# Performance work log

Hardware: AMD Instinct MI355X
Metric: run time of the kernel (lower is better)

The kernel has to match this reference:

```python
import jax, jax.numpy as jnp
import numpy as np

# ---- static config (matches init_kwargs) ----
BATCH = 8; SEQ_LEN = 1024; ENC_IN = 7; PRED_LEN = 96
D_MODEL = 512; N_HEADS = 8; D_HEAD = D_MODEL // N_HEADS
D_FF = 2048; E_LAYERS = 2; FACTOR = 5
PATCH = 16; STRIDE = 8; PAD = 8
N_PATCH = (SEQ_LEN + PAD - PATCH) // STRIDE + 1  # 128
NF = D_MODEL * N_PATCH


def _sin_pe(n, d):
    # sinusoidal positional embedding (Informer/TSLib PositionalEmbedding)
    pos = np.arange(n, dtype=np.float32)[:, None]
    div = np.exp(np.arange(0, d, 2, dtype=np.float32) * (-np.log(10000.0) / d))
    pe = np.zeros((n, d), dtype=np.float32)
    pe[:, 0::2] = np.sin(pos * div)
    pe[:, 1::2] = np.cos(pos * div)
    return jnp.asarray(pe)


def _ln(x, g, b, eps=1e-5):
    m = x.mean(-1, keepdims=True)
    v = x.var(-1, keepdims=True)
    return (x - m) / jnp.sqrt(v + eps) * g + b


def _prob_attention(q, k, v, layer_idx):
    # Informer ProbAttention, mask_flag=False. q,k,v: [B,H,L,Dh]
    B, H, L, Dh = q.shape
    u = min(int(FACTOR * np.ceil(np.log(L))), L)  # sample_k == n_top here (L_Q == L_K)
    skey = jax.random.fold_in(jax.random.key(42), layer_idx)
    samp = jax.random.randint(skey, (L, u), 0, L)          # random keys per query
    k_s = k[:, :, samp, :]                                  # [B,H,L,u,Dh]
    qk_s = jnp.einsum('bhld,bhlsd->bhls', q, k_s)           # sampled scores
    M = qk_s.max(-1) - qk_s.mean(-1)                        # sparsity measure [B,H,L]
    top = jax.lax.top_k(M, u)[1]                            # active query idx [B,H,u]
    q_r = jnp.take_along_axis(q, top[..., None], axis=2)    # [B,H,u,Dh]
    scores = jnp.einsum('bhud,bhld->bhul', q_r, k) / jnp.sqrt(jnp.asarray(Dh, q.dtype))
    attn = jax.nn.softmax(scores, axis=-1)
    upd = jnp.einsum('bhul,bhld->bhud', attn, v)            # [B,H,u,Dh]
    ctx = jnp.broadcast_to(v.mean(axis=2, keepdims=True), (B, H, L, Dh))
    bi = jnp.arange(B)[:, None, None]
    hi = jnp.arange(H)[None, :, None]
    ctx = ctx.at[bi, hi, top].set(upd)                      # scatter updated queries
    return ctx


def reference(x_enc, x_mark_enc, x_dec, x_mark_dec, patch_W,
              Wq, bq, Wk, bk, Wv, bv, Wo, bo,
              c1W, c1b, c2W, c2b, ln1g, ln1b, ln2g, ln2b,
              encg, encb, headW, headb):
    B, L, C = x_enc.shape
    # Normalize('Stat'): per-series mean/std over time
    mean = x_enc.mean(axis=1, keepdims=True)
    std = jnp.sqrt(x_enc.var(axis=1, keepdims=True) + 1e-5)
    xn = (x_enc - mean) / std
    # PatchEmbedding: [B,C,L] -> replication-pad -> unfold -> linear + pos emb
    xc = jnp.pad(xn.transpose(0, 2, 1), ((0, 0), (0, 0), (0, PAD)), mode='edge')
    idx = np.arange(N_PATCH)[:, None] * STRIDE + np.arange(PATCH)
    tok = xc[:, :, idx].reshape(B * C, N_PATCH, PATCH) @ patch_W.T  # [BC,N,dm]
    tok = tok + _sin_pe(N_PATCH, D_MODEL)
    # Transformer encoder with ProbAttention
    for l in range(E_LAYERS):
        Beff, N, _ = tok.shape
        q = (tok @ Wq[l].T + bq[l]).reshape(Beff, N, N_HEADS, D_HEAD).transpose(0, 2, 1, 3)
        k = (tok @ Wk[l].T + bk[l]).reshape(Beff, N, N_HEADS, D_HEAD).transpose(0, 2, 1, 3)
        v = (tok @ Wv[l].T + bv[l]).reshape(Beff, N, N_HEADS, D_HEAD).transpose(0, 2, 1, 3)
        ctx = _prob_attention(q, k, v, l).transpose(0, 2, 1, 3).reshape(Beff, N, D_MODEL)
        x1 = _ln(tok + ctx @ Wo[l].T + bo[l], ln1g[l], ln1b[l])
        y = jax.nn.gelu(x1 @ c1W[l].T + c1b[l], approximate=False)  # conv1d k=1 == linear
        y = y @ c2W[l].T + c2b[l]
        tok = _ln(x1 + y, ln2g[l], ln2b[l])
    tok = _ln(tok, encg, encb)
    # FlattenHead: [B,C,N,dm] -> [B,C,dm,N] -> flatten -> linear -> [B,pred,C]
    feat = tok.reshape(B, C, N_PATCH, D_MODEL).transpose(0, 1, 3, 2).reshape(B, C, NF)
    dec = (feat @ headW.T + headb).transpose(0, 2, 1)
    return dec * std + mean  # de-normalize


def setup_inputs():
    key = jax.random.key(0)
    ks = iter(jax.random.split(key, 40))
    def rn(shape, s=0.02):
        return jax.random.normal(next(ks), shape, jnp.float32) * s
    return {
        'x_enc': jax.random.normal(next(ks), (BATCH, SEQ_LEN, ENC_IN), jnp.float32),
        'x_mark_enc': jax.random.normal(next(ks), (BATCH, SEQ_LEN, 4), jnp.float32),
        'x_dec': jax.random.normal(next(ks), (BATCH, 144, ENC_IN), jnp.float32),
        'x_mark_dec': jax.random.normal(next(ks), (BATCH, 144, 4), jnp.float32),
        'patch_W': rn((D_MODEL, PATCH)),
        'Wq': rn((E_LAYERS, D_MODEL, D_MODEL)), 'bq': jnp.zeros((E_LAYERS, D_MODEL)),
        'Wk': rn((E_LAYERS, D_MODEL, D_MODEL)), 'bk': jnp.zeros((E_LAYERS, D_MODEL)),
        'Wv': rn((E_LAYERS, D_MODEL, D_MODEL)), 'bv': jnp.zeros((E_LAYERS, D_MODEL)),
        'Wo': rn((E_LAYERS, D_MODEL, D_MODEL)), 'bo': jnp.zeros((E_LAYERS, D_MODEL)),
        'c1W': rn((E_LAYERS, D_FF, D_MODEL)), 'c1b': jnp.zeros((E_LAYERS, D_FF)),
        'c2W': rn((E_LAYERS, D_MODEL, D_FF)), 'c2b': jnp.zeros((E_LAYERS, D_MODEL)),
        'ln1g': jnp.ones((E_LAYERS, D_MODEL)), 'ln1b': jnp.zeros((E_LAYERS, D_MODEL)),
        'ln2g': jnp.ones((E_LAYERS, D_MODEL)), 'ln2b': jnp.zeros((E_LAYERS, D_MODEL)),
        'encg': jnp.ones((D_MODEL,)), 'encb': jnp.zeros((D_MODEL,)),
        'headW': rn((PRED_LEN, NF)), 'headb': jnp.zeros((PRED_LEN,)),
    }
```

## Files before the change

kernel.cpp:

```cpp
#include <hip/hip_runtime.h>
#include <math.h>
#include <stdint.h>

#define SEQ   1024
#define CIN   7
#define NB    8
#define BC    56
#define NP    128
#define DM    512
#define NH    8
#define DH    64
#define DFF   2048
#define U     25
#define NTOK  (BC*NP)
#define PE_COEF (-9.210340371976184f / 512.0f)
#define HKB   256
#define HNB   256

typedef __attribute__((ext_vector_type(8))) short short8;
typedef __attribute__((ext_vector_type(4))) float f32x4;

__device__ __forceinline__ short f2bf(float x) {
    union { float f; uint32_t u; } v; v.f = x;
    uint32_t r = v.u + 0x7FFFu + ((v.u >> 16) & 1u);
    return (short)(r >> 16);
}
__device__ __forceinline__ float bf2f(short x) {
    union { uint32_t u; float f; } v; v.u = ((uint32_t)(uint16_t)x) << 16;
    return v.f;
}

__device__ __forceinline__ void gl_lds16(const void* g, void* s) {
    __builtin_amdgcn_global_load_lds((const __attribute__((address_space(1))) void*)g,
                                     (__attribute__((address_space(3))) void*)s, 16, 0, 0);
}

__global__ void stats_kernel(const float* __restrict__ x, float* __restrict__ mean,
                             float* __restrict__ stdv) {
    int bc = blockIdx.x; int b = bc / CIN, c = bc % CIN;
    const float* base = x + (size_t)b * SEQ * CIN + c;
    float s = 0.f, ss = 0.f;
    for (int i = threadIdx.x; i < SEQ; i += 256) {
        float v = base[(size_t)i * CIN];
        s += v; ss += v * v;
    }
    __shared__ float rs[256], rss[256];
    rs[threadIdx.x] = s; rss[threadIdx.x] = ss; __syncthreads();
    for (int o = 128; o > 0; o >>= 1) {
        if (threadIdx.x < o) { rs[threadIdx.x] += rs[threadIdx.x + o]; rss[threadIdx.x] += rss[threadIdx.x + o]; }
        __syncthreads();
    }
    if (threadIdx.x == 0) {
        float m = rs[0] / SEQ;
        float v = rss[0] / SEQ - m * m;
        mean[bc] = m;
        stdv[bc] = sqrtf(v + 1e-5f);
    }
}

__device__ __forceinline__ void tf_round(uint32_t& x0, uint32_t& x1, uint32_t r) {
    x0 += x1; x1 = (x1 << r) | (x1 >> (32u - r)); x1 ^= x0;
}
__device__ void threefry2x32(uint32_t k0, uint32_t k1, uint32_t x0, uint32_t x1,
                             uint32_t& o0, uint32_t& o1) {
    uint32_t ks[3] = { k0, k1, k0 ^ k1 ^ 0x1BD11BDAu };
    x0 += ks[0]; x1 += ks[1];
    const uint32_t rotA[4] = {13u, 15u, 26u, 6u}, rotB[4] = {17u, 29u, 16u, 24u};
    #pragma unroll
    for (int i = 0; i < 5; i++) {
        const uint32_t* rr = (i & 1) ? rotB : rotA;
        tf_round(x0, x1, rr[0]); tf_round(x0, x1, rr[1]);
        tf_round(x0, x1, rr[2]); tf_round(x0, x1, rr[3]);
        x0 += ks[(i + 1) % 3];
        x1 += ks[(i + 2) % 3] + (uint32_t)(i + 1);
    }
    o0 = x0; o1 = x1;
}

__global__ void prep_weights(const float* __restrict__ Wq, const float* __restrict__ Wk,
                             const float* __restrict__ Wv, const float* __restrict__ bq,
                             const float* __restrict__ bk, const float* __restrict__ bv,
                             const float* __restrict__ Wo, const float* __restrict__ c1W,
                             const float* __restrict__ c2W,
                             short* __restrict__ wqkv, float* __restrict__ bqkv,
                             short* __restrict__ wo_b, short* __restrict__ c1w_b,
                             short* __restrict__ c2w_b, int* __restrict__ samp) {
    int blk = blockIdx.x, tid = threadIdx.x;
    if (blk < 1536) {
        int idx = blk * 256 + tid;
        int k4 = idx & 127;
        int n  = (idx >> 7) % 1536;
        int l  = idx / (1536 * 128);
        int sel3 = n >> 9;
        int nn = n & 511;
        const float* src = sel3 == 0 ? Wq : sel3 == 1 ? Wk : Wv;
        float4 v = *(const float4*)(src + ((size_t)l * DM + nn) * DM + k4 * 4);
        short4 o; o.x = f2bf(v.x); o.y = f2bf(v.y); o.z = f2bf(v.z); o.w = f2bf(v.w);
        *(short4*)(wqkv + ((size_t)l * 1536 + n) * DM + k4 * 4) = o;
        if (k4 == 0) {
            const float* bsrc = sel3 == 0 ? bq : sel3 == 1 ? bk : bv;
            bqkv[l * 1536 + n] = bsrc[l * DM + nn];
        }
    } else if (blk < 6144) {
        const float* in; short* out; int i;
        if (blk < 2048)      { in = Wo;  out = wo_b;  i = (blk - 1536) * 256 + tid; }
        else if (blk < 4096) { in = c1W; out = c1w_b; i = (blk - 2048) * 256 + tid; }
        else                 { in = c2W; out = c2w_b; i = (blk - 4096) * 256 + tid; }
        float4 v = ((const float4*)in)[i];
        short4 o; o.x = f2bf(v.x); o.y = f2bf(v.y); o.z = f2bf(v.z); o.w = f2bf(v.w);
        ((short4*)out)[i] = o;
    } else {
        int l = blk - 6144;
        uint32_t s0, s1; threefry2x32(0u, 42u, 0u, (uint32_t)l, s0, s1);
        uint32_t a0, a1, b0, b1;
        threefry2x32(s0, s1, 0u, 2u, a0, a1);
        threefry2x32(s0, s1, 1u, 3u, b0, b1);
        uint32_t k20 = a1, k21 = b1;
        for (int i = tid; i < 1600; i += 256) {
            uint32_t o0, o1;
            threefry2x32(k20, k21, (uint32_t)i, (uint32_t)(1600 + i), o0, o1);
            samp[l * 3200 + i]        = (int)(o0 & 127u);
            samp[l * 3200 + 1600 + i] = (int)(o1 & 127u);
        }
    }
}

__global__ void patch_embed(const float* __restrict__ x, const float* __restrict__ pw,
                            const float* __restrict__ mean, const float* __restrict__ stdv,
                            float* __restrict__ tok, short* __restrict__ tokb) {
    int p = blockIdx.x, bc = blockIdx.y;
    int b = bc / CIN, c = bc % CIN;
    __shared__ float xs[16];
    if (threadIdx.x < 16) {
        int i = p * 8 + threadIdx.x;
        if (i > SEQ - 1) i = SEQ - 1;
        xs[threadIdx.x] = (x[(size_t)b * SEQ * CIN + (size_t)i * CIN + c] - mean[bc]) / stdv[bc];
    }
    __syncthreads();
    for (int d = threadIdx.x; d < DM; d += blockDim.x) {
        float acc = 0.f;
        const float* wr = pw + d * 16;
        #pragma unroll
        for (int t = 0; t < 16; t++) acc += xs[t] * wr[t];
        int k2 = d & ~1;
        float ang = (float)p * expf((float)k2 * PE_COEF);
        acc += (d & 1) ? cosf(ang) : sinf(ang);
        size_t idx = ((size_t)bc * NP + p) * DM + d;
        tok[idx] = acc;
        tokb[idx] = f2bf(acc);
    }
}

template<int ACT, int OBF>
__global__ __launch_bounds__(256) void gemm_mfma(const short* __restrict__ A,
                                                 const short* __restrict__ W,
                                                 const float* __restrict__ bias,
                                                 float* __restrict__ Cf,
                                                 short* __restrict__ Cb,
                                                 int M, int N, int K) {
    __shared__ short LDSU[2][16384];
    int tid = threadIdx.x;
    int w = tid >> 6, lane = tid & 63;
    int row0 = blockIdx.x * 128, col0 = blockIdx.y * 128;
    int wrow = (w >> 1) * 64, wcol = (w & 1) * 64;
    int ksub = K / gridDim.z;
    int k0 = blockIdx.z * ksub;
    int nt = ksub >> 6;
    f32x4 acc[4][4] = {};

    auto stage = [&](int b, int kt) {
        #pragma unroll
        for (int i = 0; i < 4; i++) {
            int L = i * 4096 + w * 1024 + lane * 16;
            int row = L >> 7;
            int cb  = L & 127;
            int scb = cb ^ ((row & 7) << 4);
            gl_lds16(A + (size_t)(row0 + row) * K + kt + (scb >> 1),
                     (char*)&LDSU[b][0] + i * 4096 + w * 1024);
            gl_lds16(W + (size_t)(col0 + row) * K + kt + (scb >> 1),
                     (char*)&LDSU[b][8192] + i * 4096 + w * 1024);
        }
    };

    stage(0, k0);
    __syncthreads();
    int cur = 0;
    for (int t = 0; t < nt; t++) {
        if (t + 1 < nt) stage(cur ^ 1, k0 + (t + 1) * 64);
        const char* Ab = (const char*)&LDSU[cur][0];
        const char* Bb = (const char*)&LDSU[cur][8192];
        #pragma unroll
        for (int ks = 0; ks < 2; ks++) {
            int cb = ks * 64 + ((lane >> 4) << 4);
            short8 af[4], bfr[4];
            #pragma unroll
            for (int m = 0; m < 4; m++) {
                int r = wrow + m * 16 + (lane & 15);
                af[m] = *(const short8*)(Ab + r * 128 + (cb ^ ((r & 7) << 4)));
            }
            #pragma unroll
            for (int n = 0; n < 4; n++) {
                int r = wcol + n * 16 + (lane & 15);
                bfr[n] = *(const short8*)(Bb + r * 128 + (cb ^ ((r & 7) << 4)));
            }
            #pragma unroll
            for (int m = 0; m < 4; m++)
                #pragma unroll
                for (int n = 0; n < 4; n++)
                    acc[m][n] = __builtin_amdgcn_mfma_f32_16x16x32_bf16(af[m], bfr[n], acc[m][n], 0, 0, 0);
        }
        __syncthreads();
        cur ^= 1;
    }

    float* Cfo = Cf + (size_t)blockIdx.z * M * N;
    #pragma unroll
    for (int m = 0; m < 4; m++) {
        int rbase = row0 + wrow + m * 16 + ((lane >> 4) << 2);
        #pragma unroll
        for (int n = 0; n < 4; n++) {
            int col = col0 + wcol + n * 16 + (lane & 15);
            float bval = (blockIdx.z == 0) ? bias[col] : 0.f;
            #pragma unroll
            for (int j = 0; j < 4; j++) {
                float v = acc[m][n][j] + bval;
                if (ACT == 1) {
                    float u = 0.7978845608f * (v + 0.044715f * v * v * v);
                    float e = exp2f(2.8853900817779268f * u);
                    v = v - v / (e + 1.0f);
                }
                if (OBF) Cb[(size_t)(rbase + j) * N + col] = f2bf(v);
                else     Cfo[(size_t)(rbase + j) * N + col] = v;
            }
        }
    }
}

__global__ __launch_bounds__(256, 2) void attn_fused(const short* __restrict__ qkvb,
                                                     const int* __restrict__ samp,
                                                     short* __restrict__ ctxb) {
    __shared__ float Sbuf[64 * 130];
    __shared__ short Vt[64 * 128];
    __shared__ short Kls[128 * 64];
    __shared__ float Mv[128];
    __shared__ int   topl[32];
    __shared__ float vmean[64];
    __shared__ float vpart[256];

    float* Stop = Sbuf;
    short* Pb   = (short*)(Sbuf + 32 * 130);

    int bh = blockIdx.x, bc = bh >> 3, h = bh & 7;
    int tid = threadIdx.x, w = tid >> 6, lane = tid & 63;
    const short* base = qkvb + (size_t)bc * NP * 1536 + h * DH;
    short* cbase = ctxb + (size_t)bc * NP * DM + h * DH;

    for (int e = tid; e < 1024; e += 256) {
        int row = e >> 3, c8 = e & 7;
        short8 kv = *(const short8*)(base + (size_t)row * 1536 + 512 + c8 * 8);
        *(short8*)((char*)Kls + row * 128 + ((c8 * 16) ^ ((row & 7) << 4))) = kv;
        short8 vv = *(const short8*)(base + (size_t)row * 1536 + 1024 + c8 * 8);
        #pragma unroll
        for (int j = 0; j < 8; j++) {
            int d = c8 * 8 + j;
            *(short*)((char*)Vt + d * 256 + ((2 * row) ^ ((d & 7) << 4))) = vv[j];
        }
    }
    __syncthreads();
    {
        int d = tid & 63, part = tid >> 6;
        float s = 0.f;
        #pragma unroll
        for (int i4 = 0; i4 < 4; i4++) {
            short8 v = *(const short8*)((char*)Vt + d * 256 + ((part * 64 + i4 * 16) ^ ((d & 7) << 4)));
            #pragma unroll
            for (int j = 0; j < 8; j++) s += bf2f(v[j]);
        }
        vpart[part * 64 + d] = s;
    }

    for (int half = 0; half < 2; half++) {
        int ar = half * 64 + 16 * w + (lane & 15);
        const short* qp = base + (size_t)ar * 1536;
        short8 a0 = *(const short8*)(qp + (lane >> 4) * 8);
        short8 a1 = *(const short8*)(qp + 32 + (lane >> 4) * 8);
        #pragma unroll 2
        for (int ct = 0; ct < 8; ct++) {
            int br = ct * 16 + (lane & 15);
            int cb0 = (lane >> 4) * 16;
            short8 b0 = *(const short8*)((char*)Kls + br * 128 + (cb0 ^ ((br & 7) << 4)));
            short8 b1 = *(const short8*)((char*)Kls + br * 128 + ((cb0 + 64) ^ ((br & 7) << 4)));
            f32x4 acc = {};
            acc = __builtin_amdgcn_mfma_f32_16x16x32_bf16(a0, b0, acc, 0, 0, 0);
            acc = __builtin_amdgcn_mfma_f32_16x16x32_bf16(a1, b1, acc, 0, 0, 0);
            int r0 = 16 * w + ((lane >> 4) << 2);
            int c = ct * 16 + (lane & 15);
            #pragma unroll
            for (int j = 0; j < 4; j++) Sbuf[(r0 + j) * 130 + c] = acc[j] * 0.125f;
        }
        __syncthreads();
        if (tid < 64) {
            int r = half * 64 + tid;
            const int* sp = samp + r * U;
            const float* Srow = &Sbuf[tid * 130];
            float mx = -1e30f, sm = 0.f;
            #pragma unroll
            for (int s = 0; s < U; s++) { float v = Srow[sp[s]]; mx = fmaxf(mx, v); sm += v; }
            Mv[r] = mx - sm * (1.0f / U);
        } else if (half == 0 && tid < 128) {
            int d = tid - 64;
            vmean[d] = (vpart[d] + vpart[64 + d] + vpart[128 + d] + vpart[192 + d]) * (1.0f / 128.0f);
        }
        __syncthreads();
    }

    if (w == 0) {
        float v0 = Mv[lane], v1 = Mv[lane + 64];
        for (int it = 0; it < U; it++) {
            float bv; int bi;
            if (v1 > v0) { bv = v1; bi = lane + 64; } else { bv = v0; bi = lane; }
            #pragma unroll
            for (int o = 32; o > 0; o >>= 1) {
                float ov = __shfl_xor(bv, o);
                int   oi = __shfl_xor(bi, o);
                if (ov > bv || (ov == bv && oi < bi)) { bv = ov; bi = oi; }
            }
            if (lane == 0) topl[it] = bi;
            if (bi == lane) v0 = -1e30f;
            if (bi == lane + 64) v1 = -1e30f;
        }
    } else {
        for (int e = tid - 64; e < 128 * 16; e += 192) {
            int n = e >> 4, c4 = e & 15;
            short4 o;
            o.x = f2bf(vmean[c4 * 4 + 0]); o.y = f2bf(vmean[c4 * 4 + 1]);
            o.z = f2bf(vmean[c4 * 4 + 2]); o.w = f2bf(vmean[c4 * 4 + 3]);
            *(short4*)(cbase + (size_t)n * DM + c4 * 4) = o;
        }
    }
    __syncthreads();

    {
        int rt = w & 1, cth = w >> 1;
        int u = rt * 16 + (lane & 15);
        int qrow = topl[u < U ? u : U - 1];
        const short* qp = base + (size_t)qrow * 1536;
        short8 a0 = *(const short8*)(qp + (lane >> 4) * 8);
        short8 a1 = *(const short8*)(qp + 32 + (lane >> 4) * 8);
        #pragma unroll
        for (int cti = 0; cti < 4; cti++) {
            int ct = cth * 4 + cti;
            int br = ct * 16 + (lane & 15);
            int cb0 = (lane >> 4) * 16;
            short8 b0 = *(const short8*)((char*)Kls + br * 128 + (cb0 ^ ((br & 7) << 4)));
            short8 b1 = *(const short8*)((char*)Kls + br * 128 + ((cb0 + 64) ^ ((br & 7) << 4)));
            f32x4 acc = {};
            acc = __builtin_amdgcn_mfma_f32_16x16x32_bf16(a0, b0, acc, 0, 0, 0);
            acc = __builtin_amdgcn_mfma_f32_16x16x32_bf16(a1, b1, acc, 0, 0, 0);
            int r0 = rt * 16 + ((lane >> 4) << 2);
            int c = ct * 16 + (lane & 15);
            #pragma unroll
            for (int j = 0; j < 4; j++) Stop[(r0 + j) * 130 + c] = acc[j] * 0.125f;
        }
    }
    __syncthreads();

    for (int e = tid; e < 7 * 128; e += 256)
        Pb[(25 + (e >> 7)) * 128 + (e & 127)] = 0;
    for (int it = w; it < U; it += 4) {
        float s0 = Stop[it * 130 + lane], s1 = Stop[it * 130 + 64 + lane];
        float mx = fmaxf(s0, s1);
        #pragma unroll
        for (int o = 32; o > 0; o >>= 1) mx = fmaxf(mx, __shfl_xor(mx, o));
        float e0 = expf(s0 - mx), e1 = expf(s1 - mx);
        float sum = e0 + e1;
        #pragma unroll
        for (int o = 32; o > 0; o >>= 1) sum += __shfl_xor(sum, o);
        float inv = 1.0f / sum;
        int sw = (it & 7) << 4;
        *(short*)((char*)Pb + it * 256 + ((2 * lane) ^ sw))        = f2bf(e0 * inv);
        *(short*)((char*)Pb + it * 256 + ((2 * (64 + lane)) ^ sw)) = f2bf(e1 * inv);
    }
    __syncthreads();

    #pragma unroll
    for (int t = w * 2; t < w * 2 + 2; t++) {
        int rt = t >> 2, ct = t & 3;
        int pr = rt * 16 + (lane & 15);
        int vr = ct * 16 + (lane & 15);
        f32x4 acc = {};
        #pragma unroll
        for (int ks = 0; ks < 4; ks++) {
            int off = ks * 64 + (lane >> 4) * 16;
            short8 a = *(const short8*)((char*)Pb + pr * 256 + (off ^ ((pr & 7) << 4)));
            short8 b = *(const short8*)((char*)Vt + vr * 256 + (off ^ ((vr & 7) << 4)));
            acc = __builtin_amdgcn_mfma_f32_16x16x32_bf16(a, b, acc, 0, 0, 0);
        }
        int u0 = rt * 16 + ((lane >> 4) << 2), d = ct * 16 + (lane & 15);
        #pragma unroll
        for (int j = 0; j < 4; j++) {
            int u = u0 + j;
            if (u < U) cbase[(size_t)topl[u] * DM + d] = f2bf(acc[j]);
        }
    }
}

__global__ __launch_bounds__(256) void residual_ln(const float* __restrict__ a,
                                                   const float* __restrict__ b,
                                                   const float* __restrict__ b2,
                                                   const float* __restrict__ g,
                                                   const float* __restrict__ beta,
                                                   float* __restrict__ out,
                                                   short* __restrict__ outb) {
    int row = blockIdx.x;
    int tid = threadIdx.x;
    const float* ar = a + (size_t)row * DM;
    float x0 = ar[tid], x1 = ar[tid + 256];
    if (b) {
        const float* br = b + (size_t)row * DM;
        x0 += br[tid]; x1 += br[tid + 256];
    }
    if (b2) {
        const float* br = b2 + (size_t)row * DM;
        x0 += br[tid]; x1 += br[tid + 256];
    }
    __shared__ float rs[256], rss[256];
    rs[tid] = x0 + x1; rss[tid] = x0 * x0 + x1 * x1; __syncthreads();
    for (int o = 128; o > 0; o >>= 1) {
        if (tid < o) { rs[tid] += rs[tid + o]; rss[tid] += rss[tid + o]; }
        __syncthreads();
    }
    float m = rs[0] / DM;
    float var = rss[0] / DM - m * m;
    float r = rsqrtf(var + 1e-5f);
    float y0 = (x0 - m) * r * g[tid] + beta[tid];
    float y1 = (x1 - m) * r * g[tid + 256] + beta[tid + 256];
    out[(size_t)row * DM + tid]       = y0;
    out[(size_t)row * DM + tid + 256] = y1;
    if (outb) {
        outb[(size_t)row * DM + tid]       = f2bf(y0);
        outb[(size_t)row * DM + tid + 256] = f2bf(y1);
    }
}

__global__ void transpose_tok(const float* __restrict__ tok, short* __restrict__ featb) {
    __shared__ float t[32][33];
    int bc = blockIdx.z, dt = blockIdx.y, pt = blockIdx.x;
    int tx = threadIdx.x, ty = threadIdx.y;
    #pragma unroll
    for (int i = 0; i < 4; i++) {
        int p = pt * 32 + ty + i * 8;
        int d = dt * 32 + tx;
        t[ty + i * 8][tx] = tok[((size_t)bc * NP + p) * DM + d];
    }
    __syncthreads();
    #pragma unroll
    for (int i = 0; i < 4; i++) {
        int d = dt * 32 + ty + i * 8;
        int p = pt * 32 + tx;
        featb[(size_t)bc * (DM * NP) + (size_t)d * NP + p] = f2bf(t[tx][ty + i * 8]);
    }
}

__global__ __launch_bounds__(256) void head_mfma(const float* __restrict__ hw,
                                                 const short* __restrict__ featb,
                                                 float* __restrict__ partial) {
    __shared__ short Als[96 * 64];
    __shared__ short Bls[64 * 64];
    int tid = threadIdx.x;
    int w = tid >> 6, lane = tid & 63;
    int wm = w >> 1, wn = w & 1;
    int kb = blockIdx.x * HKB;
    f32x4 acc[3][2] = {};
    const char* Ab = (const char*)Als;
    const char* Bb = (const char*)Bls;

    for (int kt = 0; kt < HKB; kt += 64) {
        #pragma unroll
        for (int i = 0; i < 6; i++) {
            int s = tid + i * 256;
            int row = s >> 4, c4 = s & 15;
            float4 v = *(const float4*)(hw + (size_t)row * 65536 + kb + kt + c4 * 4);
            short4 o; o.x = f2bf(v.x); o.y = f2bf(v.y); o.z = f2bf(v.z); o.w = f2bf(v.w);
            int boff = row * 128 + ((c4 * 8) ^ ((row & 7) << 4));
            *(short4*)((char*)Als + boff) = o;
        }
        #pragma unroll
        for (int i = 0; i < 4; i++) {
            int s = tid + i * 256;
            int row = s >> 4, c4 = s & 15;
            short4 o;
            if (row < BC) o = *(const short4*)(featb + (size_t)row * 65536 + kb + kt + c4 * 4);
            else { o.x = 0; o.y = 0; o.z = 0; o.w = 0; }
            int boff = row * 128 + ((c4 * 8) ^ ((row & 7) << 4));
            *(short4*)((char*)Bls + boff) = o;
        }
        __syncthreads();
        #pragma unroll
        for (int ks = 0; ks < 2; ks++) {
            int cb = ks * 64 + ((lane >> 4) << 4);
            short8 af[3], bfr[2];
            #pragma unroll
            for (int m = 0; m < 3; m++) {
                int r = wm * 48 + m * 16 + (lane & 15);
                af[m] = *(const short8*)(Ab + r * 128 + (cb ^ ((r & 7) << 4)));
            }
            #pragma unroll
            for (int n = 0; n < 2; n++) {
                int r = wn * 32 + n * 16 + (lane & 15);
                bfr[n] = *(const short8*)(Bb + r * 128 + (cb ^ ((r & 7) << 4)));
            }
            #pragma unroll
            for (int m = 0; m < 3; m++)
                #pragma unroll
                for (int n = 0; n < 2; n++)
                    acc[m][n] = __builtin_amdgcn_mfma_f32_16x16x32_bf16(af[m], bfr[n], acc[m][n], 0, 0, 0);
        }
        __syncthreads();
    }

    float* pb = partial + (size_t)blockIdx.x * (96 * 64);
    #pragma unroll
    for (int m = 0; m < 3; m++) {
        int rbase = wm * 48 + m * 16 + ((lane >> 4) << 2);
        #pragma unroll
        for (int n = 0; n < 2; n++) {
            int col = wn * 32 + n * 16 + (lane & 15);
            #pragma unroll
            for (int j = 0; j < 4; j++)
                pb[(rbase + j) * 64 + col] = acc[m][n][j];
        }
    }
}

__global__ void finalize_a(const float* __restrict__ partial, float* __restrict__ p2) {
    int i = blockIdx.x * 256 + threadIdx.x;
    int s = blockIdx.y;
    const float* p = partial + (size_t)s * 32 * 6144 + i;
    float sum = 0.f;
    #pragma unroll
    for (int b = 0; b < 32; b++) sum += p[(size_t)b * 6144];
    p2[s * 6144 + i] = sum;
}

__global__ void finalize_b(const float* __restrict__ p2, const float* __restrict__ hb,
                           const float* __restrict__ mean, const float* __restrict__ stdv,
                           float* __restrict__ out) {
    int i = blockIdx.x * 256 + threadIdx.x;
    if (i >= NB * 96 * CIN) return;
    int b = i / (96 * CIN);
    int r = i % (96 * CIN);
    int t = r / CIN, c = r % CIN;
    int bc = b * CIN + c;
    int j = t * 64 + bc;
    float s = 0.f;
    #pragma unroll
    for (int k = 0; k < 8; k++) s += p2[k * 6144 + j];
    out[i] = (s + hb[t]) * stdv[bc] + mean[bc];
}

extern "C" void kernel_launch(void* const* d_in, const int* in_sizes, int n_in,
                              void* d_out, int out_size, void* d_ws, size_t ws_size,
                              hipStream_t stream) {
    (void)in_sizes; (void)n_in; (void)out_size; (void)ws_size;
    const float* x_enc   = (const float*)d_in[0];
    const float* patch_W = (const float*)d_in[4];
    const float* Wq  = (const float*)d_in[5];
    const float* bq  = (const float*)d_in[6];
    const float* Wk  = (const float*)d_in[7];
    const float* bk  = (const float*)d_in[8];
    const float* Wv  = (const float*)d_in[9];
    const float* bv  = (const float*)d_in[10];
    const float* Wo  = (const float*)d_in[11];
    const float* bo  = (const float*)d_in[12];
    const float* c1W = (const float*)d_in[13];
    const float* c1b = (const float*)d_in[14];
    const float* c2W = (const float*)d_in[15];
    const float* c2b = (const float*)d_in[16];
    const float* ln1g = (const float*)d_in[17];
    const float* ln1b = (const float*)d_in[18];
    const float* ln2g = (const float*)d_in[19];
    const float* ln2b = (const float*)d_in[20];
    const float* encg = (const float*)d_in[21];
    const float* encb = (const float*)d_in[22];
    const float* headW = (const float*)d_in[23];
    const float* headb = (const float*)d_in[24];
    float* out = (float*)d_out;

    float* ws = (float*)d_ws;
    float* mean = ws + 0;
    float* stdv = ws + 64;
    float* bqkv = ws + 128;
    int*   samp = (int*)(ws + 6144);
    size_t off = 32768;
    const size_t T = (size_t)NTOK * DM;
    float* tok     = ws + off; off += T;
    float* pA      = ws + off; off += T;
    float* pB      = ws + off; off += T;
    float* x1      = ws + off; off += T;
    float* partial = ws + off; off += T;
    float* p2      = x1;
    short* sbase = (short*)(ws + off);
    size_t soff = 0;
    short* tok_b  = sbase + soff; soff += T;
    short* ctx_b  = sbase + soff; soff += T;
    short* x1_b   = sbase + soff; soff += T;
    short* qkv_b  = sbase + soff; soff += 3 * T;
    short* ffn_b  = sbase + soff; soff += (size_t)NTOK * DFF;
    short* featb  = ffn_b;
    short* wqkv_b = sbase + soff; soff += 2 * 1536 * DM;
    short* wo_b   = sbase + soff; soff += 2 * DM * DM;
    short* c1w_b  = sbase + soff; soff += 2 * (size_t)DFF * DM;
    short* c2w_b  = sbase + soff; soff += 2 * (size_t)DM * DFF;

    stats_kernel<<<BC, 256, 0, stream>>>(x_enc, mean, stdv);
    prep_weights<<<6146, 256, 0, stream>>>(Wq, Wk, Wv, bq, bk, bv, Wo, c1W, c2W,
                                           wqkv_b, bqkv, wo_b, c1w_b, c2w_b, samp);
    patch_embed<<<dim3(NP, BC), 128, 0, stream>>>(x_enc, patch_W, mean, stdv, tok, tok_b);

    for (int l = 0; l < 2; l++) {
        gemm_mfma<0,1><<<dim3(56, 12), 256, 0, stream>>>(tok_b, wqkv_b + (size_t)l * 1536 * DM, bqkv + l * 1536, nullptr, qkv_b, NTOK, 1536, DM);
        attn_fused<<<448, 256, 0, stream>>>(qkv_b, samp + l * 3200, ctx_b);
        gemm_mfma<0,0><<<dim3(56, 4, 2), 256, 0, stream>>>(ctx_b, wo_b + (size_t)l * DM * DM, bo + l * DM, pA, nullptr, NTOK, DM, DM);
        residual_ln<<<NTOK, 256, 0, stream>>>(tok, pA, pB, ln1g + l * DM, ln1b + l * DM, x1, x1_b);
        gemm_mfma<1,1><<<dim3(56, 16), 256, 0, stream>>>(x1_b, c1w_b + (size_t)l * DFF * DM, c1b + l * DFF, nullptr, ffn_b, NTOK, DFF, DM);
        gemm_mfma<0,0><<<dim3(56, 4, 2), 256, 0, stream>>>(ffn_b, c2w_b + (size_t)l * DM * DFF, c2b + l * DM, pA, nullptr, NTOK, DM, DFF);
        residual_ln<<<NTOK, 256, 0, stream>>>(x1, pA, pB, ln2g + l * DM, ln2b + l * DM, tok, tok_b);
    }

    residual_ln<<<NTOK, 256, 0, stream>>>(tok, nullptr, nullptr, encg, encb, tok, nullptr);
    transpose_tok<<<dim3(4, 16, BC), dim3(32, 8), 0, stream>>>(tok, featb);
    head_mfma<<<HNB, 256, 0, stream>>>(headW, featb, partial);
    finalize_a<<<dim3(24, 8), 256, 0, stream>>>(partial, p2);
    finalize_b<<<21, 256, 0, stream>>>(p2, headb, mean, stdv, out);
}
```

Baseline: 337.5 us.

## Replace split-K GEMMs with 64-row tile GEMM and drop partial-sum buffer

The N=512 output projections (Wo and FFN down) previously used split-K over two z-slices, writing two fp32 partial buffers that residual_ln then summed. A new 64x128 tile GEMM without split-K keeps the same block count (112x4) and writes a single output, so residual_ln reads one partial buffer instead of two. This cuts partial-buffer traffic, at the cost of each block running the full K loop serially. Patch embedding also switches to fast intrinsic exp/sin/cos, which lowers accuracy slightly.

```diff
diff --git a/kernel.cpp b/kernel.cpp
--- a/kernel.cpp
+++ b/kernel.cpp
@@ -143,8 +143,8 @@
         #pragma unroll
         for (int t = 0; t < 16; t++) acc += xs[t] * wr[t];
         int k2 = d & ~1;
-        float ang = (float)p * expf((float)k2 * PE_COEF);
-        acc += (d & 1) ? cosf(ang) : sinf(ang);
+        float ang = (float)p * __expf((float)k2 * PE_COEF);
+        acc += (d & 1) ? __cosf(ang) : __sinf(ang);
         size_t idx = ((size_t)bc * NP + p) * DM + d;
         tok[idx] = acc;
         tokb[idx] = f2bf(acc);
@@ -163,9 +163,7 @@
     int w = tid >> 6, lane = tid & 63;
     int row0 = blockIdx.x * 128, col0 = blockIdx.y * 128;
     int wrow = (w >> 1) * 64, wcol = (w & 1) * 64;
-    int ksub = K / gridDim.z;
-    int k0 = blockIdx.z * ksub;
-    int nt = ksub >> 6;
+    int nt = K >> 6;
     f32x4 acc[4][4] = {};
 
     auto stage = [&](int b, int kt) {
@@ -182,11 +180,11 @@
         }
     };
 
-    stage(0, k0);
+    stage(0, 0);
     __syncthreads();
     int cur = 0;
     for (int t = 0; t < nt; t++) {
-        if (t + 1 < nt) stage(cur ^ 1, k0 + (t + 1) * 64);
+        if (t + 1 < nt) stage(cur ^ 1, (t + 1) * 64);
         const char* Ab = (const char*)&LDSU[cur][0];
         const char* Bb = (const char*)&LDSU[cur][8192];
         #pragma unroll
@@ -213,14 +211,13 @@
         cur ^= 1;
     }
 
-    float* Cfo = Cf + (size_t)blockIdx.z * M * N;
     #pragma unroll
     for (int m = 0; m < 4; m++) {
         int rbase = row0 + wrow + m * 16 + ((lane >> 4) << 2);
         #pragma unroll
         for (int n = 0; n < 4; n++) {
             int col = col0 + wcol + n * 16 + (lane & 15);
-            float bval = (blockIdx.z == 0) ? bias[col] : 0.f;
+            float bval = bias[col];
             #pragma unroll
             for (int j = 0; j < 4; j++) {
                 float v = acc[m][n][j] + bval;
@@ -230,8 +227,84 @@
                     v = v - v / (e + 1.0f);
                 }
                 if (OBF) Cb[(size_t)(rbase + j) * N + col] = f2bf(v);
-                else     Cfo[(size_t)(rbase + j) * N + col] = v;
+                else     Cf[(size_t)(rbase + j) * N + col] = v;
             }
+        }
+    }
+}
+
+__global__ __launch_bounds__(256) void gemm_mfma64(const short* __restrict__ A,
+                                                   const short* __restrict__ W,
+                                                   const float* __restrict__ bias,
+                                                   float* __restrict__ Cf,
+                                                   int M, int N, int K) {
+    __shared__ short LDSU[2][12288];
+    int tid = threadIdx.x;
+    int w = tid >> 6, lane = tid & 63;
+    int row0 = blockIdx.x * 64, col0 = blockIdx.y * 128;
+    int nt = K >> 6;
+    f32x4 acc[4][2] = {};
+
+    auto stage = [&](int b, int kt) {
+        #pragma unroll
+        for (int i = 0; i < 2; i++) {
+            int L = (i * 4 + w) * 1024 + lane * 16;
+            int row = L >> 7, cb = L & 127;
+            int scb = cb ^ ((row & 7) << 4);
+            gl_lds16(A + (size_t)(row0 + row) * K + kt + (scb >> 1),
+                     (char*)&LDSU[b][0] + (i * 4 + w) * 1024);
+        }
+        #pragma unroll
+        for (int i = 0; i < 4; i++) {
+            int L = (i * 4 + w) * 1024 + lane * 16;
+            int row = L >> 7, cb = L & 127;
+            int scb = cb ^ ((row & 7) << 4);
+            gl_lds16(W + (size_t)(col0 + row) * K + kt + (scb >> 1),
+                     (char*)&LDSU[b][4096] + (i * 4 + w) * 1024);
+        }
+    };
+
+    stage(0, 0);
+    __syncthreads();
+    int cur = 0;
+    for (int t = 0; t < nt; t++) {
+        if (t + 1 < nt) stage(cur ^ 1, (t + 1) * 64);
+        const char* Ab = (const char*)&LDSU[cur][0];
+        const char* Bb = (const char*)&LDSU[cur][4096];
+        #pragma unroll
+        for (int ks = 0; ks < 2; ks++) {
+            int cb = ks * 64 + ((lane >> 4) << 4);
+            short8 af[4], bfr[2];
+            #pragma unroll
+            for (int m = 0; m < 4; m++) {
+                int r = m * 16 + (lane & 15);
+                af[m] = *(const short8*)(Ab + r * 128 + (cb ^ ((r & 7) << 4)));
+            }
+            #pragma unroll
+            for (int n = 0; n < 2; n++) {
+                int r = w * 32 + n * 16 + (lane & 15);
+                bfr[n] = *(const short8*)(Bb + r * 128 + (cb ^ ((r & 7) << 4)));
+            }
+            #pragma unroll
+            for (int m = 0; m < 4; m++)
+                #pragma unroll
+                for (int n = 0; n < 2; n++)
+                    acc[m][n] = __builtin_amdgcn_mfma_f32_16x16x32_bf16(af[m], bfr[n], acc[m][n], 0, 0, 0);
+        }
+        __syncthreads();
+        cur ^= 1;
+    }
+
+    #pragma unroll
+    for (int m = 0; m < 4; m++) {
+        int rbase = row0 + m * 16 + ((lane >> 4) << 2);
+        #pragma unroll
+        for (int n = 0; n < 2; n++) {
+            int col = col0 + w * 32 + n * 16 + (lane & 15);
+            float bval = bias[col];
+            #pragma unroll
+            for (int j = 0; j < 4; j++)
+                Cf[(size_t)(rbase + j) * N + col] = acc[m][n][j] + bval;
         }
     }
 }
@@ -596,7 +669,6 @@
     const size_t T = (size_t)NTOK * DM;
     float* tok     = ws + off; off += T;
     float* pA      = ws + off; off += T;
-    float* pB      = ws + off; off += T;
     float* x1      = ws + off; off += T;
     float* partial = ws + off; off += T;
     float* p2      = x1;
@@ -621,11 +693,11 @@
     for (int l = 0; l < 2; l++) {
         gemm_mfma<0,1><<<dim3(56, 12), 256, 0, stream>>>(tok_b, wqkv_b + (size_t)l * 1536 * DM, bqkv + l * 1536, nullptr, qkv_b, NTOK, 1536, DM);
         attn_fused<<<448, 256, 0, stream>>>(qkv_b, samp + l * 3200, ctx_b);
-        gemm_mfma<0,0><<<dim3(56, 4, 2), 256, 0, stream>>>(ctx_b, wo_b + (size_t)l * DM * DM, bo + l * DM, pA, nullptr, NTOK, DM, DM);
-        residual_ln<<<NTOK, 256, 0, stream>>>(tok, pA, pB, ln1g + l * DM, ln1b + l * DM, x1, x1_b);
+        gemm_mfma64<<<dim3(112, 4), 256, 0, stream>>>(ctx_b, wo_b + (size_t)l * DM * DM, bo + l * DM, pA, NTOK, DM, DM);
+        residual_ln<<<NTOK, 256, 0, stream>>>(tok, pA, nullptr, ln1g + l * DM, ln1b + l * DM, x1, x1_b);
         gemm_mfma<1,1><<<dim3(56, 16), 256, 0, stream>>>(x1_b, c1w_b + (size_t)l * DFF * DM, c1b + l * DFF, nullptr, ffn_b, NTOK, DFF, DM);
-        gemm_mfma<0,0><<<dim3(56, 4, 2), 256, 0, stream>>>(ffn_b, c2w_b + (size_t)l * DM * DFF, c2b + l * DM, pA, nullptr, NTOK, DM, DFF);
-        residual_ln<<<NTOK, 256, 0, stream>>>(x1, pA, pB, ln2g + l * DM, ln2b + l * DM, tok, tok_b);
+        gemm_mfma64<<<dim3(112, 4), 256, 0, stream>>>(ffn_b, c2w_b + (size_t)l * DM * DFF, c2b + l * DM, pA, NTOK, DM, DFF);
+        residual_ln<<<NTOK, 256, 0, stream>>>(x1, pA, nullptr, ln2g + l * DM, ln2b + l * DM, tok, tok_b);
     }
 
     residual_ln<<<NTOK, 256, 0, stream>>>(tok, nullptr, nullptr, encg, encb, tok, nullptr);
```

After: 318.0 us. 5.8% less time.
